# Optimization experiments

Hardware: AMD Instinct MI355X
Metric: run time of the kernel (lower is better)

The kernel has to match this reference:

```python
import jax, jax.numpy as jnp
import numpy as np

N = 100000
D = 100
E = 1600000


def setup_inputs() -> dict:
    key = jax.random.key(0)
    k1, k2, k3, k4 = jax.random.split(key, 4)
    embedding = jax.random.normal(k1, (N, D), dtype=jnp.float32)
    adj_rows = jax.random.randint(k2, (E,), 0, N, dtype=jnp.int32)
    adj_cols = jax.random.randint(k3, (E,), 0, N, dtype=jnp.int32)
    adj_vals = jax.random.uniform(k4, (E,), dtype=jnp.float32)
    return {
        "embedding": embedding,
        "adj_rows": adj_rows,
        "adj_cols": adj_cols,
        "adj_vals": adj_vals,
        "layer_num": 3,
    }


def _spmm(rows, cols, vals, x):
    # sparse [N,N] @ dense [N,D] via gather + weighted segment-sum scatter
    msgs = x[cols] * vals[:, None]           # [E, D]
    return jax.ops.segment_sum(msgs, rows, num_segments=N)  # [N, D]


def reference(embedding, adj_rows, adj_cols, adj_vals, layer_num):
    # out = sum_{i=0}^{layer_num} A^i x  (accumulate hops, including layer 0)
    h = embedding
    acc = embedding
    for _ in range(layer_num):
        h = _spmm(adj_rows, adj_cols, adj_vals, h)
        acc = acc + h
    return acc
```

## Files before the change

### kernel.cpp

```cpp
#include <hip/hip_runtime.h>


#define NODES 100000
#define DIM 100
#define DIM4 25
#define CH 13
#define BSHIFT 8
#define NBUCKETS ((NODES + 255) >> 8)
#define NPAD (NBUCKETS << BSHIFT)
#define TILESHIFT 13
#define NBINS 4096

typedef _Float16 half4_t __attribute__((ext_vector_type(4)));
typedef _Float16 half8_t __attribute__((ext_vector_type(8)));

__global__ void cvt_hist_kernel(const float4* __restrict__ emb, half4_t* __restrict__ x0,
                                const int* __restrict__ rows, int* __restrict__ bktCount, int E) {
    __shared__ int h[NBUCKETS];
    for (int i = threadIdx.x; i < NBUCKETS; i += blockDim.x) h[i] = 0;
    __syncthreads();
    int stride = gridDim.x * blockDim.x;
    int gid = blockIdx.x * blockDim.x + threadIdx.x;
    for (int i = gid; i < NODES * 26; i += stride) {
        int r = i / 26, c = i - r * 26;
        half4_t hv;
        if (c < 25) {
            float4 f = emb[r * 25 + c];
            hv.x = (_Float16)f.x; hv.y = (_Float16)f.y;
            hv.z = (_Float16)f.z; hv.w = (_Float16)f.w;
        } else {
            hv.x = (_Float16)0.f; hv.y = (_Float16)0.f;
            hv.z = (_Float16)0.f; hv.w = (_Float16)0.f;
        }
        x0[i] = hv;
    }
    for (int e = gid; e < E; e += stride)
        atomicAdd(&h[rows[e] >> BSHIFT], 1);
    __syncthreads();
    for (int i = threadIdx.x; i < NBUCKETS; i += blockDim.x)
        if (h[i]) atomicAdd(&bktCount[i], h[i]);
}

__global__ void bucket_scan_kernel(const int* __restrict__ bktCount,
                                   int* __restrict__ bktStart, int* __restrict__ bktCur) {
    __shared__ int s[512];
    int tid = threadIdx.x;
    int v = (tid < NBUCKETS) ? bktCount[tid] : 0;
    s[tid] = v;
    __syncthreads();
    for (int off = 1; off < 512; off <<= 1) {
        int t = (tid >= off) ? s[tid - off] : 0;
        __syncthreads();
        s[tid] += t;
        __syncthreads();
    }
    int excl = s[tid] - v;
    if (tid <= NBUCKETS) bktStart[tid] = excl;
    if (tid < NBUCKETS)  bktCur[tid]  = excl;
}

__global__ void pass1_kernel(const int* __restrict__ rows, const int* __restrict__ cols,
                             const float* __restrict__ vals,
                             int* __restrict__ bktCur, int2* __restrict__ staging, int E) {
    __shared__ int cnt[NBUCKETS];
    __shared__ int base[NBUCKETS];
    int tid = threadIdx.x;
    for (int i = tid; i < NBUCKETS; i += blockDim.x) cnt[i] = 0;
    __syncthreads();
    int chunk = (E + gridDim.x - 1) / gridDim.x;
    int s = blockIdx.x * chunk;
    int e = min(E, s + chunk);
    for (int i = s + tid; i < e; i += blockDim.x)
        atomicAdd(&cnt[rows[i] >> BSHIFT], 1);
    __syncthreads();
    for (int i = tid; i < NBUCKETS; i += blockDim.x) {
        int c = cnt[i];
        base[i] = c ? atomicAdd(&bktCur[i], c) : 0;
        cnt[i] = 0;
    }
    __syncthreads();
    for (int i = s + tid; i < e; i += blockDim.x) {
        int r = rows[i];
        int b = r >> BSHIFT;
        int pos = base[b] + atomicAdd(&cnt[b], 1);
        staging[pos] = make_int2(cols[i] | ((r & 255) << 17), __float_as_int(vals[i]));
    }
}

__global__ void pass2_kernel(const int* __restrict__ bktStart, const int2* __restrict__ staging,
                             int* __restrict__ rowstart, int2* __restrict__ csr) {
    __shared__ int hist[NBINS];
    __shared__ int psum[256];
    int b = blockIdx.x, t = threadIdx.x;
    int s = bktStart[b], e = bktStart[b + 1];
    for (int i = t; i < NBINS; i += 256) hist[i] = 0;
    __syncthreads();
    for (int i = s + t; i < e; i += 256) {
        int key = staging[i].x;
        int bin = (((key >> 17) & 255) << 4) | ((key & 0x1FFFF) >> TILESHIFT);
        atomicAdd(&hist[bin], 1);
    }
    __syncthreads();
    int loc[16];
    int run = 0;
    #pragma unroll
    for (int j = 0; j < 16; ++j) { loc[j] = run; run += hist[t * 16 + j]; }
    psum[t] = run;
    __syncthreads();
    for (int off = 1; off < 256; off <<= 1) {
        int x = (t >= off) ? psum[t - off] : 0;
        __syncthreads();
        psum[t] += x;
        __syncthreads();
    }
    int base = psum[t] - run;
    rowstart[(b << BSHIFT) + t] = s + base;
    #pragma unroll
    for (int j = 0; j < 16; ++j) hist[t * 16 + j] = base + loc[j];
    __syncthreads();
    for (int i = s + t; i < e; i += 256) {
        int2 rec = staging[i];
        int bin = (((rec.x >> 17) & 255) << 4) | ((rec.x & 0x1FFFF) >> TILESHIFT);
        int p = atomicAdd(&hist[bin], 1);
        csr[s + p] = make_int2(rec.x & 0x1FFFF, rec.y);
    }
}

__global__ void gather_mid_kernel(const int* __restrict__ rowstart,
                                  const int2* __restrict__ csr,
                                  const half8_t* __restrict__ x,
                                  half8_t* __restrict__ h) {
    int gid = blockIdx.x * blockDim.x + threadIdx.x;
    int row = gid >> 4, lane = gid & 15;
    if (row >= NODES || lane >= CH) return;
    int s = rowstart[row], e = rowstart[row + 1];
    float acc[8] = {0.f, 0.f, 0.f, 0.f, 0.f, 0.f, 0.f, 0.f};
    int i = s;
    for (; i + 3 < e; i += 4) {
        int2 r0 = csr[i], r1 = csr[i + 1], r2 = csr[i + 2], r3 = csr[i + 3];
        half8_t a0 = x[(size_t)r0.x * CH + lane];
        half8_t a1 = x[(size_t)r1.x * CH + lane];
        half8_t a2 = x[(size_t)r2.x * CH + lane];
        half8_t a3 = x[(size_t)r3.x * CH + lane];
        float v0 = __int_as_float(r0.y), v1 = __int_as_float(r1.y);
        float v2 = __int_as_float(r2.y), v3 = __int_as_float(r3.y);
        #pragma unroll
        for (int k = 0; k < 8; ++k)
            acc[k] += v0 * (float)a0[k] + v1 * (float)a1[k]
                    + v2 * (float)a2[k] + v3 * (float)a3[k];
    }
    for (; i < e; ++i) {
        int2 r0 = csr[i];
        half8_t a0 = x[(size_t)r0.x * CH + lane];
        float v0 = __int_as_float(r0.y);
        #pragma unroll
        for (int k = 0; k < 8; ++k) acc[k] += v0 * (float)a0[k];
    }
    half8_t hv;
    #pragma unroll
    for (int k = 0; k < 8; ++k) hv[k] = (_Float16)acc[k];
    h[(size_t)row * CH + lane] = hv;
}

__global__ void gather_last_kernel(const int* __restrict__ rowstart,
                                   const int2* __restrict__ csr,
                                   const half8_t* __restrict__ x,
                                   const half8_t* __restrict__ h1,
                                   const half8_t* __restrict__ h2,
                                   const float4* __restrict__ emb,
                                   float4* __restrict__ out) {
    int gid = blockIdx.x * blockDim.x + threadIdx.x;
    int row = gid >> 4, lane = gid & 15;
    if (row >= NODES || lane >= CH) return;
    int s = rowstart[row], e = rowstart[row + 1];
    float acc[8] = {0.f, 0.f, 0.f, 0.f, 0.f, 0.f, 0.f, 0.f};
    int i = s;
    for (; i + 3 < e; i += 4) {
        int2 r0 = csr[i], r1 = csr[i + 1], r2 = csr[i + 2], r3 = csr[i + 3];
        half8_t a0 = x[(size_t)r0.x * CH + lane];
        half8_t a1 = x[(size_t)r1.x * CH + lane];
        half8_t a2 = x[(size_t)r2.x * CH + lane];
        half8_t a3 = x[(size_t)r3.x * CH + lane];
        float v0 = __int_as_float(r0.y), v1 = __int_as_float(r1.y);
        float v2 = __int_as_float(r2.y), v3 = __int_as_float(r3.y);
        #pragma unroll
        for (int k = 0; k < 8; ++k)
            acc[k] += v0 * (float)a0[k] + v1 * (float)a1[k]
                    + v2 * (float)a2[k] + v3 * (float)a3[k];
    }
    for (; i < e; ++i) {
        int2 r0 = csr[i];
        half8_t a0 = x[(size_t)r0.x * CH + lane];
        float v0 = __int_as_float(r0.y);
        #pragma unroll
        for (int k = 0; k < 8; ++k) acc[k] += v0 * (float)a0[k];
    }
    size_t pidx = (size_t)row * CH + lane;
    half8_t a1 = h1[pidx], a2 = h2[pidx];
    int f4 = row * DIM4 + lane * 2;
    float4 o0 = emb[f4];
    o0.x += acc[0] + (float)a1[0] + (float)a2[0];
    o0.y += acc[1] + (float)a1[1] + (float)a2[1];
    o0.z += acc[2] + (float)a1[2] + (float)a2[2];
    o0.w += acc[3] + (float)a1[3] + (float)a2[3];
    out[f4] = o0;
    if (lane < 12) {
        float4 o1 = emb[f4 + 1];
        o1.x += acc[4] + (float)a1[4] + (float)a2[4];
        o1.y += acc[5] + (float)a1[5] + (float)a2[5];
        o1.z += acc[6] + (float)a1[6] + (float)a2[6];
        o1.w += acc[7] + (float)a1[7] + (float)a2[7];
        out[f4 + 1] = o1;
    }
}

extern "C" void kernel_launch(void* const* d_in, const int* in_sizes, int n_in,
                              void* d_out, int out_size, void* d_ws, size_t ws_size,
                              hipStream_t stream) {
    const float* emb  = (const float*)d_in[0];
    const int*   rows = (const int*)  d_in[1];
    const int*   cols = (const int*)  d_in[2];
    const float* vals = (const float*)d_in[3];
    const int E = in_sizes[1];

    const size_t ndp_bytes = (size_t)NODES * 104 * sizeof(_Float16);

    char* w = (char*)d_ws;
    half8_t* x0p      = (half8_t*)w;  w += ndp_bytes;
    half8_t* h1p      = (half8_t*)w;  w += ndp_bytes;
    half8_t* h2p      = (half8_t*)w;  w += ndp_bytes;
    int2*    staging  = (int2*)   w;  w += (size_t)E * sizeof(int2);
    int2*    csr      = (int2*)   w;  w += (size_t)E * sizeof(int2);
    int*     rowstart = (int*)    w;  w += (size_t)(NPAD + 256) * sizeof(int);
    int*     bktCount = (int*)    w;  w += 512 * sizeof(int);
    int*     bktStart = (int*)    w;  w += 512 * sizeof(int);
    int*     bktCur   = (int*)    w;  w += 512 * sizeof(int);

    float4* out = (float4*)d_out;

    hipMemsetAsync(bktCount, 0, NBUCKETS * sizeof(int), stream);
    cvt_hist_kernel<<<1024, 256, 0, stream>>>((const float4*)emb, (half4_t*)x0p,
                                              rows, bktCount, E);
    bucket_scan_kernel<<<1, 512, 0, stream>>>(bktCount, bktStart, bktCur);
    pass1_kernel<<<256, 256, 0, stream>>>(rows, cols, vals, bktCur, staging, E);
    pass2_kernel<<<NBUCKETS, 256, 0, stream>>>(bktStart, staging, rowstart, csr);

    const long long threads = (long long)NODES * 16;
    dim3 gGrid((unsigned)((threads + 255) / 256)), gBlock(256);
    gather_mid_kernel<<<gGrid, gBlock, 0, stream>>>(rowstart, csr, x0p, h1p);
    gather_mid_kernel<<<gGrid, gBlock, 0, stream>>>(rowstart, csr, h1p, h2p);
    gather_last_kernel<<<gGrid, gBlock, 0, stream>>>(rowstart, csr, h2p, h1p, h2p,
                                                     (const float4*)emb, out);
}
```

Baseline: 394.9 us.

## Fold bucket scan into pass1, simplify row sort, unroll second gather by eight

The separate single-block bucket scan is removed: each pass1 block recomputes the bucket prefix sum in shared memory and adds a per-bucket atomic cursor. Pass2 now sorts only by local row instead of by row plus column tile, and both passes use 512-thread blocks. The second hop uses a new gather kernel that unrolls eight edges per iteration for more loads in flight. The final kernel adds the fp16 copy of the embedding instead of reading the fp32 input, which cuts traffic but lowers precision of the layer-0 term. Dropping the column-tile ordering may hurt gather locality.

```diff
diff --git a/kernel.cpp b/kernel.cpp
--- a/kernel.cpp
+++ b/kernel.cpp
@@ -8,8 +8,6 @@
 #define BSHIFT 8
 #define NBUCKETS ((NODES + 255) >> 8)
 #define NPAD (NBUCKETS << BSHIFT)
-#define TILESHIFT 13
-#define NBINS 4096
 
 typedef _Float16 half4_t __attribute__((ext_vector_type(4)));
 typedef _Float16 half8_t __attribute__((ext_vector_type(8)));
@@ -41,95 +39,88 @@
         if (h[i]) atomicAdd(&bktCount[i], h[i]);
 }
 
-__global__ void bucket_scan_kernel(const int* __restrict__ bktCount,
-                                   int* __restrict__ bktStart, int* __restrict__ bktCur) {
-    __shared__ int s[512];
-    int tid = threadIdx.x;
-    int v = (tid < NBUCKETS) ? bktCount[tid] : 0;
-    s[tid] = v;
-    __syncthreads();
-    for (int off = 1; off < 512; off <<= 1) {
-        int t = (tid >= off) ? s[tid - off] : 0;
-        __syncthreads();
-        s[tid] += t;
-        __syncthreads();
-    }
-    int excl = s[tid] - v;
-    if (tid <= NBUCKETS) bktStart[tid] = excl;
-    if (tid < NBUCKETS)  bktCur[tid]  = excl;
-}
-
 __global__ void pass1_kernel(const int* __restrict__ rows, const int* __restrict__ cols,
                              const float* __restrict__ vals,
-                             int* __restrict__ bktCur, int2* __restrict__ staging, int E) {
+                             const int* __restrict__ bktCount, int* __restrict__ gCur,
+                             int* __restrict__ bktStart,
+                             int2* __restrict__ staging, int E) {
     __shared__ int cnt[NBUCKETS];
-    __shared__ int base[NBUCKETS];
-    int tid = threadIdx.x;
-    for (int i = tid; i < NBUCKETS; i += blockDim.x) cnt[i] = 0;
+    __shared__ int bst[NBUCKETS];
+    __shared__ int sc[512];
+    int t = threadIdx.x;
+    for (int i = t; i < NBUCKETS; i += 512) cnt[i] = 0;
     __syncthreads();
     int chunk = (E + gridDim.x - 1) / gridDim.x;
     int s = blockIdx.x * chunk;
     int e = min(E, s + chunk);
-    for (int i = s + tid; i < e; i += blockDim.x)
+    for (int i = s + t; i < e; i += 512)
         atomicAdd(&cnt[rows[i] >> BSHIFT], 1);
-    __syncthreads();
-    for (int i = tid; i < NBUCKETS; i += blockDim.x) {
-        int c = cnt[i];
-        base[i] = c ? atomicAdd(&bktCur[i], c) : 0;
-        cnt[i] = 0;
-    }
-    __syncthreads();
-    for (int i = s + tid; i < e; i += blockDim.x) {
+    int v = (t < NBUCKETS) ? bktCount[t] : 0;
+    sc[t] = v;
+    __syncthreads();
+    for (int off = 1; off < 512; off <<= 1) {
+        int x = (t >= off) ? sc[t - off] : 0;
+        __syncthreads();
+        sc[t] += x;
+        __syncthreads();
+    }
+    int excl = sc[t] - v;
+    if (blockIdx.x == 0) {
+        if (t < NBUCKETS) bktStart[t] = excl;
+        if (t == 0) bktStart[NBUCKETS] = E;
+    }
+    if (t < NBUCKETS) {
+        int c = cnt[t];
+        bst[t] = excl + (c ? atomicAdd(&gCur[t], c) : 0);
+        cnt[t] = 0;
+    }
+    __syncthreads();
+    for (int i = s + t; i < e; i += 512) {
         int r = rows[i];
         int b = r >> BSHIFT;
-        int pos = base[b] + atomicAdd(&cnt[b], 1);
+        int pos = bst[b] + atomicAdd(&cnt[b], 1);
         staging[pos] = make_int2(cols[i] | ((r & 255) << 17), __float_as_int(vals[i]));
     }
 }
 
 __global__ void pass2_kernel(const int* __restrict__ bktStart, const int2* __restrict__ staging,
                              int* __restrict__ rowstart, int2* __restrict__ csr) {
-    __shared__ int hist[NBINS];
-    __shared__ int psum[256];
+    __shared__ int hist[256];
+    __shared__ int cur[256];
     int b = blockIdx.x, t = threadIdx.x;
     int s = bktStart[b], e = bktStart[b + 1];
-    for (int i = t; i < NBINS; i += 256) hist[i] = 0;
-    __syncthreads();
-    for (int i = s + t; i < e; i += 256) {
-        int key = staging[i].x;
-        int bin = (((key >> 17) & 255) << 4) | ((key & 0x1FFFF) >> TILESHIFT);
-        atomicAdd(&hist[bin], 1);
-    }
-    __syncthreads();
-    int loc[16];
-    int run = 0;
-    #pragma unroll
-    for (int j = 0; j < 16; ++j) { loc[j] = run; run += hist[t * 16 + j]; }
-    psum[t] = run;
+    if (t < 256) hist[t] = 0;
+    __syncthreads();
+    for (int i = s + t; i < e; i += 512)
+        atomicAdd(&hist[(staging[i].x >> 17) & 255], 1);
+    __syncthreads();
+    int v = (t < 256) ? hist[t] : 0;
+    if (t < 256) cur[t] = v;
     __syncthreads();
     for (int off = 1; off < 256; off <<= 1) {
-        int x = (t >= off) ? psum[t - off] : 0;
-        __syncthreads();
-        psum[t] += x;
-        __syncthreads();
-    }
-    int base = psum[t] - run;
-    rowstart[(b << BSHIFT) + t] = s + base;
-    #pragma unroll
-    for (int j = 0; j < 16; ++j) hist[t * 16 + j] = base + loc[j];
-    __syncthreads();
-    for (int i = s + t; i < e; i += 256) {
+        int x = (t >= off && t < 256) ? cur[t - off] : 0;
+        __syncthreads();
+        if (t < 256) cur[t] += x;
+        __syncthreads();
+    }
+    if (t < 256) {
+        int excl = cur[t] - v;
+        rowstart[(b << BSHIFT) + t] = s + excl;
+        hist[t] = excl;
+    }
+    __syncthreads();
+    for (int i = s + t; i < e; i += 512) {
         int2 rec = staging[i];
-        int bin = (((rec.x >> 17) & 255) << 4) | ((rec.x & 0x1FFFF) >> TILESHIFT);
-        int p = atomicAdd(&hist[bin], 1);
+        int lr = (rec.x >> 17) & 255;
+        int p = atomicAdd(&hist[lr], 1);
         csr[s + p] = make_int2(rec.x & 0x1FFFF, rec.y);
     }
 }
 
-__global__ void gather_mid_kernel(const int* __restrict__ rowstart,
-                                  const int2* __restrict__ csr,
-                                  const half8_t* __restrict__ x,
-                                  half8_t* __restrict__ h) {
+__global__ void gather_mid4_kernel(const int* __restrict__ rowstart,
+                                   const int2* __restrict__ csr,
+                                   const half8_t* __restrict__ x,
+                                   half8_t* __restrict__ h) {
     int gid = blockIdx.x * blockDim.x + threadIdx.x;
     int row = gid >> 4, lane = gid & 15;
     if (row >= NODES || lane >= CH) return;
@@ -162,12 +153,49 @@
     h[(size_t)row * CH + lane] = hv;
 }
 
+__global__ void gather_mid8_kernel(const int* __restrict__ rowstart,
+                                   const int2* __restrict__ csr,
+                                   const half8_t* __restrict__ x,
+                                   half8_t* __restrict__ h) {
+    int gid = blockIdx.x * blockDim.x + threadIdx.x;
+    int row = gid >> 4, lane = gid & 15;
+    if (row >= NODES || lane >= CH) return;
+    int s = rowstart[row], e = rowstart[row + 1];
+    float acc[8] = {0.f, 0.f, 0.f, 0.f, 0.f, 0.f, 0.f, 0.f};
+    int i = s;
+    for (; i + 7 < e; i += 8) {
+        int2 rr[8];
+        #pragma unroll
+        for (int j = 0; j < 8; ++j) rr[j] = csr[i + j];
+        half8_t aa[8];
+        #pragma unroll
+        for (int j = 0; j < 8; ++j) aa[j] = x[(size_t)rr[j].x * CH + lane];
+        #pragma unroll
+        for (int j = 0; j < 8; ++j) {
+            float v = __int_as_float(rr[j].y);
+            #pragma unroll
+            for (int k = 0; k < 8; ++k) acc[k] += v * (float)aa[j][k];
+        }
+    }
+    for (; i < e; ++i) {
+        int2 r0 = csr[i];
+        half8_t a0 = x[(size_t)r0.x * CH + lane];
+        float v0 = __int_as_float(r0.y);
+        #pragma unroll
+        for (int k = 0; k < 8; ++k) acc[k] += v0 * (float)a0[k];
+    }
+    half8_t hv;
+    #pragma unroll
+    for (int k = 0; k < 8; ++k) hv[k] = (_Float16)acc[k];
+    h[(size_t)row * CH + lane] = hv;
+}
+
 __global__ void gather_last_kernel(const int* __restrict__ rowstart,
                                    const int2* __restrict__ csr,
                                    const half8_t* __restrict__ x,
+                                   const half8_t* __restrict__ x0,
                                    const half8_t* __restrict__ h1,
                                    const half8_t* __restrict__ h2,
-                                   const float4* __restrict__ emb,
                                    float4* __restrict__ out) {
     int gid = blockIdx.x * blockDim.x + threadIdx.x;
     int row = gid >> 4, lane = gid & 15;
@@ -196,20 +224,20 @@
         for (int k = 0; k < 8; ++k) acc[k] += v0 * (float)a0[k];
     }
     size_t pidx = (size_t)row * CH + lane;
-    half8_t a1 = h1[pidx], a2 = h2[pidx];
+    half8_t xe = x0[pidx], a1 = h1[pidx], a2 = h2[pidx];
     int f4 = row * DIM4 + lane * 2;
-    float4 o0 = emb[f4];
-    o0.x += acc[0] + (float)a1[0] + (float)a2[0];
-    o0.y += acc[1] + (float)a1[1] + (float)a2[1];
-    o0.z += acc[2] + (float)a1[2] + (float)a2[2];
-    o0.w += acc[3] + (float)a1[3] + (float)a2[3];
+    float4 o0;
+    o0.x = acc[0] + (float)xe[0] + (float)a1[0] + (float)a2[0];
+    o0.y = acc[1] + (float)xe[1] + (float)a1[1] + (float)a2[1];
+    o0.z = acc[2] + (float)xe[2] + (float)a1[2] + (float)a2[2];
+    o0.w = acc[3] + (float)xe[3] + (float)a1[3] + (float)a2[3];
     out[f4] = o0;
     if (lane < 12) {
-        float4 o1 = emb[f4 + 1];
-        o1.x += acc[4] + (float)a1[4] + (float)a2[4];
-        o1.y += acc[5] + (float)a1[5] + (float)a2[5];
-        o1.z += acc[6] + (float)a1[6] + (float)a2[6];
-        o1.w += acc[7] + (float)a1[7] + (float)a2[7];
+        float4 o1;
+        o1.x = acc[4] + (float)xe[4] + (float)a1[4] + (float)a2[4];
+        o1.y = acc[5] + (float)xe[5] + (float)a1[5] + (float)a2[5];
+        o1.z = acc[6] + (float)xe[6] + (float)a1[6] + (float)a2[6];
+        o1.w = acc[7] + (float)xe[7] + (float)a1[7] + (float)a2[7];
         out[f4 + 1] = o1;
     }
 }
@@ -233,22 +261,21 @@
     int2*    csr      = (int2*)   w;  w += (size_t)E * sizeof(int2);
     int*     rowstart = (int*)    w;  w += (size_t)(NPAD + 256) * sizeof(int);
     int*     bktCount = (int*)    w;  w += 512 * sizeof(int);
+    int*     gCur     = (int*)    w;  w += 512 * sizeof(int);
     int*     bktStart = (int*)    w;  w += 512 * sizeof(int);
-    int*     bktCur   = (int*)    w;  w += 512 * sizeof(int);
 
     float4* out = (float4*)d_out;
 
-    hipMemsetAsync(bktCount, 0, NBUCKETS * sizeof(int), stream);
+    hipMemsetAsync(bktCount, 0, 1024 * sizeof(int), stream);
     cvt_hist_kernel<<<1024, 256, 0, stream>>>((const float4*)emb, (half4_t*)x0p,
                                               rows, bktCount, E);
-    bucket_scan_kernel<<<1, 512, 0, stream>>>(bktCount, bktStart, bktCur);
-    pass1_kernel<<<256, 256, 0, stream>>>(rows, cols, vals, bktCur, staging, E);
-    pass2_kernel<<<NBUCKETS, 256, 0, stream>>>(bktStart, staging, rowstart, csr);
+    pass1_kernel<<<256, 512, 0, stream>>>(rows, cols, vals, bktCount, gCur, bktStart,
+                                          staging, E);
+    pass2_kernel<<<NBUCKETS, 512, 0, stream>>>(bktStart, staging, rowstart, csr);
 
     const long long threads = (long long)NODES * 16;
     dim3 gGrid((unsigned)((threads + 255) / 256)), gBlock(256);
-    gather_mid_kernel<<<gGrid, gBlock, 0, stream>>>(rowstart, csr, x0p, h1p);
-    gather_mid_kernel<<<gGrid, gBlock, 0, stream>>>(rowstart, csr, h1p, h2p);
-    gather_last_kernel<<<gGrid, gBlock, 0, stream>>>(rowstart, csr, h2p, h1p, h2p,
-                                                     (const float4*)emb, out);
-}
+    gather_mid4_kernel<<<gGrid, gBlock, 0, stream>>>(rowstart, csr, x0p, h1p);
+    gather_mid8_kernel<<<gGrid, gBlock, 0, stream>>>(rowstart, csr, h1p, h2p);
+    gather_last_kernel<<<gGrid, gBlock, 0, stream>>>(rowstart, csr, h2p, x0p, h1p, h2p, out);
+}
```

Result: faster. 378.4 us (-4.2%).
